# Performance work log

Measured on AMD Instinct MI355X. Metric: run time of the kernel, lower is better.

## Reference

```python
import jax, jax.numpy as jnp
import numpy as np

B, IN, H, G, WR = 8192, 1024, 1024, 2, 64
UR = [64, 64]


def setup_inputs() -> dict:
    key = jax.random.key(0)
    ks = jax.random.split(key, 9)
    hg = H // G
    return {
        "x": jax.random.normal(ks[0], (B, IN), jnp.float32),
        "h": jax.random.normal(ks[1], (B, H), jnp.float32),
        "c": jax.random.normal(ks[2], (B, H), jnp.float32),
        "u_x": 0.1 * jax.random.normal(ks[3], (IN, WR), jnp.float32),
        "v_x": 0.1 * jax.random.normal(ks[4], (4 * H, WR), jnp.float32),
        "u_h_0": 0.1 * jax.random.normal(ks[5], (G, hg, UR[0]), jnp.float32),
        "v_h_0": 0.1 * jax.random.normal(ks[6], (G, UR[0], 4 * hg), jnp.float32),
        "u_h_1": 0.1 * jax.random.normal(ks[7], (G, hg, UR[1]), jnp.float32),
        "v_h_1": 0.1 * jax.random.normal(ks[8], (G, UR[1], 4 * hg), jnp.float32),
        "bias_x": jnp.ones((1, 4 * H), jnp.float32),
        "bias_h": jnp.ones((1, 4 * H), jnp.float32),
    }


def reference(x, h, c, u_x, v_x, u_h_0, v_h_0, u_h_1, v_h_1, bias_x, bias_h):
    b = h.shape[0]
    hg = H // G
    # input-to-hidden low-rank projection: [B, 4H]
    gx = (x @ u_x) @ v_x.T + bias_x
    xf, xi, xn, xo = jnp.split(gx, 4, axis=1)  # each [B, H]

    hv = h.reshape(b, G, hg)  # [B, G, H/G]
    u_hs = [u_h_0, u_h_1]
    v_hs = [v_h_0, v_h_1]
    acc = None
    for i in range(G):
        # torch code rotates the group index list cumulatively each step:
        # step i uses permutation roll(arange(G), -i)
        perm = np.roll(np.arange(G), -i)
        h_op = hv[:, perm, :]  # [B, G, hg]
        t = jnp.einsum('bgd,gdr->bgr', h_op, u_hs[i])  # [B, G, r_i]
        t = jnp.einsum('bgr,grk->bgk', t, v_hs[i])     # [B, G, 4hg]
        acc = t if acc is None else acc + t

    # chunk along last dim into 4 gates, flatten group dim -> [B, H]
    f_h, i_h, n_h, o_h = [p.reshape(b, H) for p in jnp.split(acc, 4, axis=2)]
    hf, hi, hn, ho = jnp.split(bias_h, 4, axis=1)

    inputgate = jax.nn.sigmoid(xi + hi + i_h)
    forgetgate = jax.nn.sigmoid(xf + hf + f_h)
    outputgate = jax.nn.sigmoid(xo + ho + o_h)
    newgate = jnp.tanh(xn + hn + n_h)
    c_next = forgetgate * c + inputgate * newgate
    h_next = outputgate * jnp.tanh(c_next)
    return (h_next, c_next)
```

## Files before the change

kernel.cpp:

```cpp
#include <hip/hip_runtime.h>
#include <hip/hip_bf16.h>


typedef __bf16 bf16_t;
typedef __bf16 bf16x4 __attribute__((ext_vector_type(4)));
typedef __bf16 bf16x8 __attribute__((ext_vector_type(8)));
typedef float f32x4 __attribute__((ext_vector_type(4)));

#define MFMA16x16x32(a, b, c) __builtin_amdgcn_mfma_f32_16x16x32_bf16((a), (b), (c), 0, 0, 0)

#define TA_OFF 0
#define BX_OFF 5242880
#define BH_OFF 5373952
#define BW_OFF 5636096

__device__ inline float fast_sigmoid(float x) {
  return __builtin_amdgcn_rcpf(1.f + __expf(-x));
}
__device__ inline float fast_tanh(float x) {
  return 2.f * __builtin_amdgcn_rcpf(1.f + __expf(-2.f * x)) - 1.f;
}

__global__ __launch_bounds__(256) void prep_kernel(
    const float* __restrict__ u_x, const float* __restrict__ u_h_0,
    const float* __restrict__ u_h_1, const float* __restrict__ v_h_0,
    const float* __restrict__ v_h_1, const float* __restrict__ v_x,
    bf16_t* __restrict__ Bx, bf16_t* __restrict__ Bh,
    bf16_t* __restrict__ Bw) {
  int t = blockIdx.x * 256 + threadIdx.x;
  int lane = t & 63;
  int lo = lane & 15, quad = lane >> 4;
  if (t < 8192) {
    int kk = (t >> 6) & 31, tt = t >> 11;
    int k0 = kk * 32 + quad * 8;
    const float* src = u_x + 16 * tt + lo;
    bf16x8 v;
#pragma unroll
    for (int j = 0; j < 8; ++j) v[j] = (bf16_t)src[(size_t)(k0 + j) * 64];
    *(bf16x8*)(Bx + (size_t)t * 8) = v;
  } else if (t < 24576) {
    int o2 = t - 8192;
    int kk = (o2 >> 6) & 15, sub = (o2 >> 10) & 3, s = o2 >> 12;
    int d0 = kk * 32 + quad * 8;
    const float* src =
        ((s & 1) ? u_h_1 : u_h_0) + (size_t)(s >> 1) * 32768 + 16 * sub + lo;
    bf16x8 v;
#pragma unroll
    for (int j = 0; j < 8; ++j) v[j] = (bf16_t)src[(size_t)(d0 + j) * 64];
    *(bf16x8*)(Bh + (size_t)o2 * 8) = v;
  } else {
    int t3 = t - 24576;
    int chunk = t3 >> 6;
    int ks = chunk % 6, rowt = chunk / 6;
    int gq = rowt >> 3, nt = rowt & 7;
    int gg = gq >> 4, qt = gq & 15;
    int row = 16 * nt + lo;
    int w = row >> 5, ql = row & 31;
    int k0 = ks * 32 + quad * 8;
    int m = gg * 512 + qt * 32 + ql;
    int q = qt * 32 + ql;
    bf16x8 v;
    if (ks < 2) {
      const float4* p = (const float4*)(v_x + (size_t)(w * 1024 + m) * 64 + k0);
      float4 va = p[0], vb = p[1];
      v[0] = (bf16_t)va.x; v[1] = (bf16_t)va.y;
      v[2] = (bf16_t)va.z; v[3] = (bf16_t)va.w;
      v[4] = (bf16_t)vb.x; v[5] = (bf16_t)vb.y;
      v[6] = (bf16_t)vb.z; v[7] = (bf16_t)vb.w;
    } else if (ks < 4) {
      const float* src = v_h_0 + (size_t)gg * 131072 +
                         (size_t)(k0 - 64) * 2048 + w * 512 + q;
#pragma unroll
      for (int j = 0; j < 8; ++j) v[j] = (bf16_t)src[(size_t)j * 2048];
    } else {
      const float* src = v_h_1 + (size_t)gg * 131072 +
                         (size_t)(k0 - 128) * 2048 + w * 512 + q;
#pragma unroll
      for (int j = 0; j < 8; ++j) v[j] = (bf16_t)src[(size_t)j * 2048];
    }
    *(bf16x8*)(Bw + (size_t)t3 * 8) = v;
  }
}

__global__ __launch_bounds__(512) void phase1_kernel(
    const float* __restrict__ x, const float* __restrict__ h,
    const bf16_t* __restrict__ Bx, const bf16_t* __restrict__ Bh,
    bf16_t* __restrict__ TA) {
  __shared__ bf16_t z[16][2072];
  __shared__ bf16_t pre[16][328];
  const int b0 = blockIdx.x * 16;
  const int tid = threadIdx.x;
  const int wv = tid >> 6, lane = tid & 63;
  const int lo = lane & 15, quad = lane >> 4;
  const int srow = tid >> 5, sc = tid & 31;

  {
    const float* srcx = x + (size_t)(b0 + srow) * 1024 + sc * 4;
    const float* srch = h + (size_t)(b0 + srow) * 1024 + sc * 4;
#pragma unroll
    for (int j = 0; j < 8; ++j) {
      float4 v = *(const float4*)(srcx + j * 128);
      bf16x4 pk;
      pk[0] = (bf16_t)v.x; pk[1] = (bf16_t)v.y;
      pk[2] = (bf16_t)v.z; pk[3] = (bf16_t)v.w;
      *(bf16x4*)&z[srow][sc * 4 + j * 128] = pk;
    }
#pragma unroll
    for (int j = 0; j < 8; ++j) {
      float4 v = *(const float4*)(srch + j * 128);
      bf16x4 pk;
      pk[0] = (bf16_t)v.x; pk[1] = (bf16_t)v.y;
      pk[2] = (bf16_t)v.z; pk[3] = (bf16_t)v.w;
      *(bf16x4*)&z[srow][1024 + sc * 4 + j * 128] = pk;
    }
  }
  __syncthreads();

  if (wv < 4) {
    f32x4 accx = {0.f, 0.f, 0.f, 0.f};
    const bf16_t* bx = Bx + ((size_t)(wv * 32) * 64 + lane) * 8;
    for (int kk = 0; kk < 32; ++kk) {
      bf16x8 af = *(const bf16x8*)&z[lo][kk * 32 + quad * 8];
      bf16x8 bfr = *(const bf16x8*)(bx + (size_t)kk * 512);
      accx = MFMA16x16x32(af, bfr, accx);
    }
#pragma unroll
    for (int r = 0; r < 4; ++r) pre[quad * 4 + r][16 * wv + lo] = (bf16_t)accx[r];

    const int u = 12 + wv;
    f32x4 acch = {0.f, 0.f, 0.f, 0.f};
    const bf16_t* bh = Bh + ((size_t)(u * 16) * 64 + lane) * 8;
    for (int kk = 0; kk < 16; ++kk) {
      bf16x8 af = *(const bf16x8*)&z[lo][1024 + kk * 32 + quad * 8];
      bf16x8 bfr = *(const bf16x8*)(bh + (size_t)kk * 512);
      acch = MFMA16x16x32(af, bfr, acch);
    }
#pragma unroll
    for (int r = 0; r < 4; ++r)
      pre[quad * 4 + r][64 + u * 16 + lo] = (bf16_t)acch[r];
  } else {
    const int ub = (wv - 4) * 3;
    f32x4 acc[3];
#pragma unroll
    for (int i = 0; i < 3; ++i) acc[i] = (f32x4){0.f, 0.f, 0.f, 0.f};
    int hoffA[3];
#pragma unroll
    for (int i = 0; i < 3; ++i) {
      int s = (ub + i) >> 2;
      hoffA[i] = 1024 + ((s == 1 || s == 2) ? 512 : 0);
    }
    const bf16_t* bh = Bh + ((size_t)(ub * 16) * 64 + lane) * 8;
    for (int kk = 0; kk < 16; ++kk) {
#pragma unroll
      for (int i = 0; i < 3; ++i) {
        bf16x8 af = *(const bf16x8*)&z[lo][hoffA[i] + kk * 32 + quad * 8];
        bf16x8 bfr = *(const bf16x8*)(bh + ((size_t)i * 16 + kk) * 512);
        acc[i] = MFMA16x16x32(af, bfr, acc[i]);
      }
    }
#pragma unroll
    for (int i = 0; i < 3; ++i)
#pragma unroll
      for (int r = 0; r < 4; ++r)
        pre[quad * 4 + r][64 + (ub + i) * 16 + lo] = (bf16_t)acc[i][r];
  }
  __syncthreads();

#pragma unroll
  for (int it = 0; it < 2; ++it) {
    int slot = it * 512 + tid;
    if (slot < 640) {
      int cc = slot >> 6, ln = slot & 63;
      int llo = ln & 15, lq = ln >> 4;
      bf16x8 v = *(const bf16x8*)&pre[llo][cc * 32 + lq * 8];
      *(bf16x8*)(TA + (((size_t)blockIdx.x * 10 + cc) * 64 + ln) * 8) = v;
    }
  }
}

__global__ __launch_bounds__(512, 2) void phase2_kernel(
    const bf16_t* __restrict__ TA, const bf16_t* __restrict__ Bw,
    const float* __restrict__ bias_x, const float* __restrict__ bias_h,
    const float* __restrict__ c, float* __restrict__ out) {
  __shared__ bf16_t bs[3072 * 8];

  const int b0 = blockIdx.x * 256;
  const int gq = blockIdx.y;
  const int g = gq >> 4, qt = gq & 15;
  const int tid = threadIdx.x;
  const int wv = tid >> 6, lane = tid & 63;
  const int lo = lane & 15, quad = lane >> 4;

  bf16x8 a[2][6];
#pragma unroll
  for (int mt = 0; mt < 2; ++mt) {
    int rt = blockIdx.x * 16 + wv * 2 + mt;
#pragma unroll
    for (int ks = 0; ks < 6; ++ks) {
      int cc = (ks < 2) ? ks : (g * 4 + ks);
      a[mt][ks] = *(const bf16x8*)(TA + (((size_t)rt * 10 + cc) * 64 + lane) * 8);
    }
  }

  {
    const bf16_t* src = Bw + (size_t)gq * 24576;
#pragma unroll
    for (int cch = 0; cch < 6; ++cch) {
      int ch = cch * 512 + tid;
      *(bf16x8*)&bs[(size_t)ch * 8] = *(const bf16x8*)(src + (size_t)ch * 8);
    }
  }

  float cin[2][4][2];
#pragma unroll
  for (int mt = 0; mt < 2; ++mt)
#pragma unroll
    for (int r = 0; r < 4; ++r) {
      int b = b0 + wv * 32 + mt * 16 + quad * 4 + r;
#pragma unroll
      for (int cq = 0; cq < 2; ++cq) {
        int m = g * 512 + qt * 32 + cq * 16 + lo;
        cin[mt][r][cq] = c[(size_t)b * 1024 + m];
      }
    }
  float bsum[4][2];
#pragma unroll
  for (int w = 0; w < 4; ++w)
#pragma unroll
    for (int cq = 0; cq < 2; ++cq) {
      int n = w * 1024 + g * 512 + qt * 32 + cq * 16 + lo;
      bsum[w][cq] = bias_x[n] + bias_h[n];
    }
  __syncthreads();

  f32x4 acc[2][8];
#pragma unroll
  for (int mt = 0; mt < 2; ++mt)
#pragma unroll
    for (int nt = 0; nt < 8; ++nt) acc[mt][nt] = (f32x4){0.f, 0.f, 0.f, 0.f};

#pragma unroll
  for (int nt = 0; nt < 8; ++nt) {
#pragma unroll
    for (int ks = 0; ks < 6; ++ks) {
      bf16x8 bfr = *(const bf16x8*)&bs[(size_t)(((nt * 6 + ks) << 6) + lane) * 8];
      acc[0][nt] = MFMA16x16x32(a[0][ks], bfr, acc[0][nt]);
      acc[1][nt] = MFMA16x16x32(a[1][ks], bfr, acc[1][nt]);
    }
  }

#pragma unroll
  for (int mt = 0; mt < 2; ++mt)
#pragma unroll
    for (int r = 0; r < 4; ++r) {
      int b = b0 + wv * 32 + mt * 16 + quad * 4 + r;
#pragma unroll
      for (int cq = 0; cq < 2; ++cq) {
        int m = g * 512 + qt * 32 + cq * 16 + lo;
        float fv = acc[mt][0 + cq][r] + bsum[0][cq];
        float iv = acc[mt][2 + cq][r] + bsum[1][cq];
        float nv = acc[mt][4 + cq][r] + bsum[2][cq];
        float ov = acc[mt][6 + cq][r] + bsum[3][cq];
        float ig = fast_sigmoid(iv);
        float fg = fast_sigmoid(fv);
        float og = fast_sigmoid(ov);
        float ng = fast_tanh(nv);
        float cn = fg * cin[mt][r][cq] + ig * ng;
        float hn = og * fast_tanh(cn);
        out[(size_t)b * 1024 + m] = hn;
        out[8388608ull + (size_t)b * 1024 + m] = cn;
      }
    }
}

extern "C" void kernel_launch(void* const* d_in, const int* in_sizes, int n_in,
                              void* d_out, int out_size, void* d_ws,
                              size_t ws_size, hipStream_t stream) {
  const float* x = (const float*)d_in[0];
  const float* h = (const float*)d_in[1];
  const float* c = (const float*)d_in[2];
  const float* u_x = (const float*)d_in[3];
  const float* v_x = (const float*)d_in[4];
  const float* u_h_0 = (const float*)d_in[5];
  const float* v_h_0 = (const float*)d_in[6];
  const float* u_h_1 = (const float*)d_in[7];
  const float* v_h_1 = (const float*)d_in[8];
  const float* bias_x = (const float*)d_in[9];
  const float* bias_h = (const float*)d_in[10];

  char* ws = (char*)d_ws;
  bf16_t* TA = (bf16_t*)(ws + TA_OFF);
  bf16_t* Bx = (bf16_t*)(ws + BX_OFF);
  bf16_t* Bh = (bf16_t*)(ws + BH_OFF);
  bf16_t* Bw = (bf16_t*)(ws + BW_OFF);

  prep_kernel<<<480, 256, 0, stream>>>(u_x, u_h_0, u_h_1, v_h_0, v_h_1, v_x,
                                       Bx, Bh, Bw);
  phase1_kernel<<<512, 512, 0, stream>>>(x, h, Bx, Bh, TA);
  phase2_kernel<<<dim3(32, 32), 512, 0, stream>>>(TA, Bw, bias_x, bias_h, c,
                                                  (float*)d_out);
}
```

Before: 194.9 us.

## Process four output tiles per phase2 block with double-buffered weight prefetch

```diff
diff --git a/kernel.cpp b/kernel.cpp
--- a/kernel.cpp
+++ b/kernel.cpp
@@ -182,11 +182,12 @@
     const bf16_t* __restrict__ TA, const bf16_t* __restrict__ Bw,
     const float* __restrict__ bias_x, const float* __restrict__ bias_h,
     const float* __restrict__ c, float* __restrict__ out) {
-  __shared__ bf16_t bs[3072 * 8];
+  __shared__ bf16_t bs[2][3072 * 8];
 
   const int b0 = blockIdx.x * 256;
-  const int gq = blockIdx.y;
-  const int g = gq >> 4, qt = gq & 15;
+  const int yy = blockIdx.y;
+  const int g = yy >> 2;
+  const int qtq = yy & 3;
   const int tid = threadIdx.x;
   const int wv = tid >> 6, lane = tid & 63;
   const int lo = lane & 15, quad = lane >> 4;
@@ -203,74 +204,135 @@
   }
 
   {
-    const bf16_t* src = Bw + (size_t)gq * 24576;
+    const bf16_t* src = Bw + (size_t)(g * 16 + qtq * 4) * 24576;
 #pragma unroll
     for (int cch = 0; cch < 6; ++cch) {
       int ch = cch * 512 + tid;
-      *(bf16x8*)&bs[(size_t)ch * 8] = *(const bf16x8*)(src + (size_t)ch * 8);
-    }
-  }
-
+      *(bf16x8*)&bs[0][(size_t)ch * 8] = *(const bf16x8*)(src + (size_t)ch * 8);
+    }
+  }
+
+  float bsum[4][2];
   float cin[2][4][2];
-#pragma unroll
-  for (int mt = 0; mt < 2; ++mt)
-#pragma unroll
-    for (int r = 0; r < 4; ++r) {
-      int b = b0 + wv * 32 + mt * 16 + quad * 4 + r;
+  {
+    const int qt = qtq * 4;
+#pragma unroll
+    for (int w = 0; w < 4; ++w)
 #pragma unroll
       for (int cq = 0; cq < 2; ++cq) {
-        int m = g * 512 + qt * 32 + cq * 16 + lo;
-        cin[mt][r][cq] = c[(size_t)b * 1024 + m];
-      }
-    }
-  float bsum[4][2];
-#pragma unroll
-  for (int w = 0; w < 4; ++w)
-#pragma unroll
-    for (int cq = 0; cq < 2; ++cq) {
-      int n = w * 1024 + g * 512 + qt * 32 + cq * 16 + lo;
-      bsum[w][cq] = bias_x[n] + bias_h[n];
-    }
+        int n = w * 1024 + g * 512 + qt * 32 + cq * 16 + lo;
+        bsum[w][cq] = bias_x[n] + bias_h[n];
+      }
+#pragma unroll
+    for (int mt = 0; mt < 2; ++mt)
+#pragma unroll
+      for (int r = 0; r < 4; ++r) {
+        int b = b0 + wv * 32 + mt * 16 + quad * 4 + r;
+#pragma unroll
+        for (int cq = 0; cq < 2; ++cq) {
+          int m = g * 512 + qt * 32 + cq * 16 + lo;
+          cin[mt][r][cq] = c[(size_t)b * 1024 + m];
+        }
+      }
+  }
   __syncthreads();
 
-  f32x4 acc[2][8];
-#pragma unroll
-  for (int mt = 0; mt < 2; ++mt)
-#pragma unroll
-    for (int nt = 0; nt < 8; ++nt) acc[mt][nt] = (f32x4){0.f, 0.f, 0.f, 0.f};
-
-#pragma unroll
-  for (int nt = 0; nt < 8; ++nt) {
-#pragma unroll
-    for (int ks = 0; ks < 6; ++ks) {
-      bf16x8 bfr = *(const bf16x8*)&bs[(size_t)(((nt * 6 + ks) << 6) + lane) * 8];
-      acc[0][nt] = MFMA16x16x32(a[0][ks], bfr, acc[0][nt]);
-      acc[1][nt] = MFMA16x16x32(a[1][ks], bfr, acc[1][nt]);
-    }
-  }
-
-#pragma unroll
-  for (int mt = 0; mt < 2; ++mt)
-#pragma unroll
-    for (int r = 0; r < 4; ++r) {
-      int b = b0 + wv * 32 + mt * 16 + quad * 4 + r;
-#pragma unroll
-      for (int cq = 0; cq < 2; ++cq) {
-        int m = g * 512 + qt * 32 + cq * 16 + lo;
-        float fv = acc[mt][0 + cq][r] + bsum[0][cq];
-        float iv = acc[mt][2 + cq][r] + bsum[1][cq];
-        float nv = acc[mt][4 + cq][r] + bsum[2][cq];
-        float ov = acc[mt][6 + cq][r] + bsum[3][cq];
-        float ig = fast_sigmoid(iv);
-        float fg = fast_sigmoid(fv);
-        float og = fast_sigmoid(ov);
-        float ng = fast_tanh(nv);
-        float cn = fg * cin[mt][r][cq] + ig * ng;
-        float hn = og * fast_tanh(cn);
-        out[(size_t)b * 1024 + m] = hn;
-        out[8388608ull + (size_t)b * 1024 + m] = cn;
-      }
-    }
+#pragma unroll
+  for (int p = 0; p < 4; ++p) {
+    const int qt = qtq * 4 + p;
+    const int cur = p & 1;
+
+    bf16x8 sv[6];
+    if (p < 3) {
+      const bf16_t* src = Bw + (size_t)(g * 16 + qt + 1) * 24576;
+#pragma unroll
+      for (int cch = 0; cch < 6; ++cch)
+        sv[cch] = *(const bf16x8*)(src + (size_t)(cch * 512 + tid) * 8);
+    }
+
+    f32x4 acc[2][8];
+#pragma unroll
+    for (int mt = 0; mt < 2; ++mt)
+#pragma unroll
+      for (int nt = 0; nt < 8; ++nt) acc[mt][nt] = (f32x4){0.f, 0.f, 0.f, 0.f};
+#pragma unroll
+    for (int nt = 0; nt < 8; ++nt) {
+#pragma unroll
+      for (int ks = 0; ks < 6; ++ks) {
+        bf16x8 bfr = *(const bf16x8*)&bs[cur][
+            (size_t)(((nt * 6 + ks) << 6) + lane) * 8];
+        acc[0][nt] = MFMA16x16x32(a[0][ks], bfr, acc[0][nt]);
+        acc[1][nt] = MFMA16x16x32(a[1][ks], bfr, acc[1][nt]);
+      }
+    }
+
+    if (p < 3) {
+#pragma unroll
+      for (int cch = 0; cch < 6; ++cch)
+        *(bf16x8*)&bs[cur ^ 1][(size_t)(cch * 512 + tid) * 8] = sv[cch];
+    }
+
+    float bsumN[4][2];
+    float cinN[2][4][2];
+    if (p < 3) {
+      const int qn = qt + 1;
+#pragma unroll
+      for (int w = 0; w < 4; ++w)
+#pragma unroll
+        for (int cq = 0; cq < 2; ++cq) {
+          int n = w * 1024 + g * 512 + qn * 32 + cq * 16 + lo;
+          bsumN[w][cq] = bias_x[n] + bias_h[n];
+        }
+#pragma unroll
+      for (int mt = 0; mt < 2; ++mt)
+#pragma unroll
+        for (int r = 0; r < 4; ++r) {
+          int b = b0 + wv * 32 + mt * 16 + quad * 4 + r;
+#pragma unroll
+          for (int cq = 0; cq < 2; ++cq) {
+            int m = g * 512 + qn * 32 + cq * 16 + lo;
+            cinN[mt][r][cq] = c[(size_t)b * 1024 + m];
+          }
+        }
+    }
+
+#pragma unroll
+    for (int mt = 0; mt < 2; ++mt)
+#pragma unroll
+      for (int r = 0; r < 4; ++r) {
+        int b = b0 + wv * 32 + mt * 16 + quad * 4 + r;
+#pragma unroll
+        for (int cq = 0; cq < 2; ++cq) {
+          int m = g * 512 + qt * 32 + cq * 16 + lo;
+          float fv = acc[mt][0 + cq][r] + bsum[0][cq];
+          float iv = acc[mt][2 + cq][r] + bsum[1][cq];
+          float nv = acc[mt][4 + cq][r] + bsum[2][cq];
+          float ov = acc[mt][6 + cq][r] + bsum[3][cq];
+          float ig = fast_sigmoid(iv);
+          float fg = fast_sigmoid(fv);
+          float og = fast_sigmoid(ov);
+          float ng = fast_tanh(nv);
+          float cn = fg * cin[mt][r][cq] + ig * ng;
+          float hn = og * fast_tanh(cn);
+          out[(size_t)b * 1024 + m] = hn;
+          out[8388608ull + (size_t)b * 1024 + m] = cn;
+        }
+      }
+
+    if (p < 3) {
+      __syncthreads();
+#pragma unroll
+      for (int w = 0; w < 4; ++w)
+#pragma unroll
+        for (int cq = 0; cq < 2; ++cq) bsum[w][cq] = bsumN[w][cq];
+#pragma unroll
+      for (int mt = 0; mt < 2; ++mt)
+#pragma unroll
+        for (int r = 0; r < 4; ++r)
+#pragma unroll
+          for (int cq = 0; cq < 2; ++cq) cin[mt][r][cq] = cinN[mt][r][cq];
+    }
+  }
 }
 
 extern "C" void kernel_launch(void* const* d_in, const int* in_sizes, int n_in,
@@ -297,6 +359,6 @@
   prep_kernel<<<480, 256, 0, stream>>>(u_x, u_h_0, u_h_1, v_h_0, v_h_1, v_x,
                                        Bx, Bh, Bw);
   phase1_kernel<<<512, 512, 0, stream>>>(x, h, Bx, Bh, TA);
-  phase2_kernel<<<dim3(32, 32), 512, 0, stream>>>(TA, Bw, bias_x, bias_h, c,
-                                                  (float*)d_out);
-}
+  phase2_kernel<<<dim3(32, 8), 512, 0, stream>>>(TA, Bw, bias_x, bias_h, c,
+                                                 (float*)d_out);
+}
```

Result: slower. 205.1 us (+5.2%).
